# Kernel optimization log

Measured on AMD Instinct MI355X. Metric: run time of the kernel, lower is better.

Reference implementation:

```python
import jax, jax.numpy as jnp
import numpy as np

K_IN, K_OUT, K_STATE = 32, 32, 1024
BATCH, SEQ = 64, 512


def setup_inputs() -> dict:
    key = jax.random.key(0)
    ks = jax.random.split(key, 10)
    stdv = 1.0 / np.sqrt(K_STATE)
    u = lambda k, shape: jax.random.uniform(k, shape, jnp.float32, -stdv, stdv)
    return {
        "inputs": jax.random.normal(ks[0], (BATCH, SEQ, K_IN), jnp.float32),
        "state0": jnp.zeros((K_STATE,), jnp.float32),
        "W_e": u(ks[1], (K_STATE, K_IN)),
        "b_e": u(ks[2], (K_STATE,)),
        "W_ih": u(ks[3], (3 * K_STATE, K_STATE)),
        "b_ih": u(ks[4], (3 * K_STATE,)),
        "W_hh": u(ks[5], (3 * K_STATE, K_STATE)),
        "b_hh": u(ks[6], (3 * K_STATE,)),
        "W_ly": u(ks[7], (K_OUT, K_STATE)),
    }


def reference(inputs, state0, W_e, b_e, W_ih, b_ih, W_hh, b_hh, W_ly):
    # inputs: (B, T, k_in). interpol='constant' => x_half/x_full are unused by GRUCell.
    B, T, _ = inputs.shape
    H = W_hh.shape[1]
    # expand_input: tanh(Linear(k_in -> k_state)), batched over all timesteps
    xe = jnp.tanh(jnp.einsum('btk,hk->bth', inputs, W_e) + b_e)  # (B,T,H)
    # precompute input-side GRU gate projections in one big matmul
    xp = jnp.einsum('bth,gh->btg', xe, W_ih) + b_ih  # (B,T,3H)
    h0 = jnp.broadcast_to(state0, (B, H))

    def step(h, xp_t):
        gh = h @ W_hh.T + b_hh  # (B,3H)
        xr, xz, xn = jnp.split(xp_t, 3, axis=-1)
        hr, hz, hn = jnp.split(gh, 3, axis=-1)
        r = jax.nn.sigmoid(xr + hr)
        z = jax.nn.sigmoid(xz + hz)
        n = jnp.tanh(xn + r * hn)
        h_new = (1.0 - z) * n + z * h
        return h_new, h_new

    _, hs = jax.lax.scan(step, h0, jnp.swapaxes(xp, 0, 1))  # hs: (T,B,H)
    states = jnp.swapaxes(hs, 0, 1)  # (B,T,H)
    outputs = jnp.einsum('bth,oh->bto', states, W_ly)  # (B,T,k_out)
    return outputs, states
```

## Files before the change

kernel.cpp:

```cpp
#include <hip/hip_runtime.h>
#include <hip/hip_bf16.h>
#include <stdint.h>

typedef short short8 __attribute__((ext_vector_type(8)));
typedef float f32x4 __attribute__((ext_vector_type(4)));
typedef unsigned short u16;

__device__ __forceinline__ float bf2f(u16 b){ unsigned u = ((unsigned)b) << 16; float f; __builtin_memcpy(&f, &u, 4); return f; }
__device__ __forceinline__ u16 f2bf(float f){ unsigned u; __builtin_memcpy(&u, &f, 4); u = (u + 0x7fffu + ((u >> 16) & 1u)) >> 16; return (u16)u; }
__device__ __forceinline__ float sigm(float x){ return 1.f / (1.f + __expf(-x)); }
__device__ __forceinline__ float tanh_(float x){ float e = __expf(2.f * x); return 1.f - 2.f / (e + 1.f); }

__device__ __forceinline__ short8 ld_cohx4(const u16* p){
  short8 d;
  asm volatile("global_load_dwordx4 %0, %1, off sc0 sc1" : "=v"(d) : "v"(p) : "memory");
  return d;
}
__device__ __forceinline__ int ld_coh_u32(const int* p){
  int d;
  asm volatile("global_load_dword %0, %1, off sc0 sc1" : "=v"(d) : "v"(p) : "memory");
  return d;
}
__device__ __forceinline__ void st_coh_u16(u16* p, u16 v){
  asm volatile("global_store_short %0, %1, off sc0 sc1" :: "v"(p), "v"(v) : "memory");
}
__device__ __forceinline__ void st_coh_u32(int* p, int v){
  asm volatile("global_store_dword %0, %1, off sc0 sc1" :: "v"(p), "v"(v) : "memory");
}
__device__ __forceinline__ void wait_vm0(){ asm volatile("s_waitcnt vmcnt(0)" ::: "memory"); }

__global__ __launch_bounds__(256) void k_init(const float* __restrict__ Wih, const float* __restrict__ Whh,
                                              const float* __restrict__ s0,
                                              u16* __restrict__ Wihb, u16* __restrict__ Whhb,
                                              u16* __restrict__ hslab, int* __restrict__ flags)
{
  int i = blockIdx.x * 256 + threadIdx.x;
  int n = 3072 * 1024;
  for (int idx = i; idx < n; idx += gridDim.x * 256){
    Wihb[idx] = f2bf(Wih[idx]);
    Whhb[idx] = f2bf(Whh[idx]);
  }
  if (i < 65536){
    int k = ((i >> 8) & 63) * 16 + (i & 15);
    hslab[65536 + i] = f2bf(s0[k]);
  }
  if (i < 4 * 512 * 64) flags[i] = 0;
}

__global__ __launch_bounds__(256) void k_xe(const float* __restrict__ inp, const float* __restrict__ We,
                                            const float* __restrict__ be, u16* __restrict__ xe)
{
  __shared__ float si[64][32];
  size_t m0 = (size_t)blockIdx.x * 64;
  int tid = threadIdx.x;
  for (int i = tid; i < 2048; i += 256)
    si[i >> 5][i & 31] = inp[m0 * 32 + i];
  __syncthreads();
  #pragma unroll
  for (int jj = 0; jj < 4; ++jj){
    int j = jj * 256 + tid;
    f32x4 wr[8];
    #pragma unroll
    for (int q = 0; q < 8; ++q)
      wr[q] = *(const f32x4*)(We + (size_t)j * 32 + q * 4);
    float bias = be[j];
    for (int mi = 0; mi < 64; ++mi){
      float acc = bias;
      #pragma unroll
      for (int q = 0; q < 8; ++q){
        f32x4 x = *(const f32x4*)(&si[mi][q * 4]);
        acc += x[0]*wr[q][0] + x[1]*wr[q][1] + x[2]*wr[q][2] + x[3]*wr[q][3];
      }
      xe[(m0 + mi) * 1024 + j] = f2bf(tanh_(acc));
    }
  }
}

__global__ __launch_bounds__(256) void k_xp(const u16* __restrict__ A, const u16* __restrict__ Bw,
                                            const float* __restrict__ bias, u16* __restrict__ C)
{
  __shared__ u16 As[128 * 32];
  __shared__ u16 Bs[128 * 32];
  int tid = threadIdx.x, lane = tid & 63, wv = tid >> 6;
  int wr = wv >> 1, wc = wv & 1;
  int l15 = lane & 15, l4 = lane >> 4;
  int bid = blockIdx.x;
  int mb = bid / 24, nb = bid % 24;
  int m0 = mb * 128, n0 = nb * 128;

  int srow = lane >> 2, skk = (lane & 3) * 8;
  const u16* Ab = A + ((size_t)m0 + wv * 32 + srow) * 1024 + skk;
  const u16* Bb = Bw + ((size_t)n0 + wv * 32 + srow) * 1024 + skk;

  f32x4 acc[4][4] = {};
  for (int k0 = 0; k0 < 1024; k0 += 32){
    __syncthreads();
    __builtin_amdgcn_global_load_lds(Ab + k0,              &As[(wv * 2)     * 512], 16, 0, 0);
    __builtin_amdgcn_global_load_lds(Ab + k0 + 16 * 1024,  &As[(wv * 2 + 1) * 512], 16, 0, 0);
    __builtin_amdgcn_global_load_lds(Bb + k0,              &Bs[(wv * 2)     * 512], 16, 0, 0);
    __builtin_amdgcn_global_load_lds(Bb + k0 + 16 * 1024,  &Bs[(wv * 2 + 1) * 512], 16, 0, 0);
    __syncthreads();
    short8 af[4], bf[4];
    #pragma unroll
    for (int i = 0; i < 4; ++i){
      af[i] = *(const short8*)(As + (size_t)(wr * 64 + i * 16 + l15) * 32 + l4 * 8);
      bf[i] = *(const short8*)(Bs + (size_t)(wc * 64 + i * 16 + l15) * 32 + l4 * 8);
    }
    #pragma unroll
    for (int i = 0; i < 4; ++i)
      #pragma unroll
      for (int j = 0; j < 4; ++j)
        acc[i][j] = __builtin_amdgcn_mfma_f32_16x16x32_bf16(af[i], bf[j], acc[i][j], 0, 0, 0);
  }
  #pragma unroll
  for (int j = 0; j < 4; ++j){
    int n = n0 + wc * 64 + j * 16 + l15;
    float bv = bias[n];
    #pragma unroll
    for (int i = 0; i < 4; ++i){
      int mrow = m0 + wr * 64 + i * 16 + l4 * 4;
      #pragma unroll
      for (int r = 0; r < 4; ++r)
        C[(size_t)(mrow + r) * 3072 + n] = f2bf(acc[i][j][r] + bv);
    }
  }
}

__global__ __launch_bounds__(256, 1) void k_rec(const u16* __restrict__ Whhb, const float* __restrict__ bhh,
                                                const u16* __restrict__ xpb, const float* __restrict__ s0,
                                                u16* __restrict__ hslab, float* __restrict__ states,
                                                int* __restrict__ flags)
{
  int w = blockIdx.x;
  int g = w & 3;
  int s = w >> 2;
  int jb = s * 16;
  int tid = threadIdx.x, lane = tid & 63, wv = tid >> 6;
  int l15 = lane & 15, l4 = lane >> 4;

  short8 wreg[3][8];
  #pragma unroll
  for (int gt = 0; gt < 3; ++gt){
    const u16* wp = Whhb + (size_t)(gt * 1024 + jb + l15) * 1024 + wv * 256 + l4 * 8;
    #pragma unroll
    for (int ks = 0; ks < 8; ++ks)
      wreg[gt][ks] = *(const short8*)(wp + ks * 32);
  }
  float bb0 = bhh[jb + l15], bb1 = bhh[1024 + jb + l15], bb2 = bhh[2048 + jb + l15];
  float hreg[4];
  { float v = s0[jb + l15]; hreg[0] = hreg[1] = hreg[2] = hreg[3] = v; }

  __shared__ f32x4 part[3][3][64];

  for (int t = 0; t < 512; ++t){
    u16 xq[12];
    if (wv == 0){
      #pragma unroll
      for (int gt = 0; gt < 3; ++gt)
        #pragma unroll
        for (int r = 0; r < 4; ++r){
          int b = g * 16 + l4 * 4 + r;
          xq[gt * 4 + r] = xpb[((size_t)b * 512 + t) * 3072 + gt * 1024 + jb + l15];
        }
    }
    if (t > 0){
      const int* fp_ = flags + ((size_t)g * 512 + (t - 1)) * 64 + wv * 16 + l15;
      while (true){
        int v = ld_coh_u32(fp_);
        wait_vm0();
        if (__all(v != 0)) break;
        __builtin_amdgcn_s_sleep(1);
      }
      __builtin_amdgcn_sched_barrier(0);
    }
    int rbuf = (t & 1) ^ 1;
    const char* hs = (const char*)hslab + (((size_t)rbuf * 4 + g) * 64 + wv * 16) * 512;
    const char* hl = hs + l15 * 32 + (l4 & 1) * 16;
    short8 af[8];
    #pragma unroll
    for (int ks = 0; ks < 8; ++ks)
      af[ks] = ld_cohx4((const u16*)(hl + (ks * 2 + (l4 >> 1)) * 512));
    wait_vm0();
    __builtin_amdgcn_sched_barrier(0);
    f32x4 a0 = {}, a1 = {}, a2 = {};
    #pragma unroll
    for (int ks = 0; ks < 8; ++ks){
      a0 = __builtin_amdgcn_mfma_f32_16x16x32_bf16(af[ks], wreg[0][ks], a0, 0, 0, 0);
      a1 = __builtin_amdgcn_mfma_f32_16x16x32_bf16(af[ks], wreg[1][ks], a1, 0, 0, 0);
      a2 = __builtin_amdgcn_mfma_f32_16x16x32_bf16(af[ks], wreg[2][ks], a2, 0, 0, 0);
    }
    if (wv){
      part[wv - 1][0][lane] = a0;
      part[wv - 1][1][lane] = a1;
      part[wv - 1][2][lane] = a2;
    }
    __syncthreads();
    if (wv == 0){
      f32x4 g0 = a0 + part[0][0][lane] + part[1][0][lane] + part[2][0][lane];
      f32x4 g1 = a1 + part[0][1][lane] + part[1][1][lane] + part[2][1][lane];
      f32x4 g2 = a2 + part[0][2][lane] + part[1][2][lane] + part[2][2][lane];
      int wb = t & 1;
      float hn_[4];
      #pragma unroll
      for (int r = 0; r < 4; ++r){
        float rr = sigm(bf2f(xq[r])      + g0[r] + bb0);
        float zz = sigm(bf2f(xq[4 + r])  + g1[r] + bb1);
        float nn = tanh_(bf2f(xq[8 + r]) + rr * (g2[r] + bb2));
        hn_[r] = (1.f - zz) * nn + zz * hreg[r];
        hreg[r] = hn_[r];
      }
      u16* hw = hslab + (((size_t)wb * 4 + g) * 64 + s) * 256;
      #pragma unroll
      for (int r = 0; r < 4; ++r)
        st_coh_u16(hw + (l4 * 4 + r) * 16 + l15, f2bf(hn_[r]));
      wait_vm0();
      if (lane == 0)
        st_coh_u32(flags + ((size_t)g * 512 + t) * 64 + s, 1);
      #pragma unroll
      for (int r = 0; r < 4; ++r)
        states[((size_t)(g * 16 + l4 * 4 + r) * 512 + t) * 1024 + jb + l15] = hn_[r];
    }
  }
}

__global__ __launch_bounds__(256) void k_out(const float* __restrict__ st, const float* __restrict__ Wly,
                                             float* __restrict__ out)
{
  __shared__ float srow[8][1024];
  size_t m0 = (size_t)blockIdx.x * 8;
  int tid = threadIdx.x;
  for (int i = tid; i < 8 * 1024; i += 256)
    srow[i >> 10][i & 1023] = st[(m0 + (i >> 10)) * 1024 + (i & 1023)];
  __syncthreads();
  int mi = tid >> 5, o = tid & 31;
  const float* wp = Wly + (size_t)o * 1024;
  float acc = 0.f;
  #pragma unroll 4
  for (int k = 0; k < 1024; k += 4){
    f32x4 w = *(const f32x4*)(wp + k);
    f32x4 x = *(const f32x4*)(&srow[mi][k]);
    acc += x[0]*w[0] + x[1]*w[1] + x[2]*w[2] + x[3]*w[3];
  }
  out[(m0 + mi) * 32 + o] = acc;
}

extern "C" void kernel_launch(void* const* d_in, const int* in_sizes, int n_in,
                              void* d_out, int out_size, void* d_ws, size_t ws_size,
                              hipStream_t stream)
{
  const float* inputs = (const float*)d_in[0];
  const float* s0     = (const float*)d_in[1];
  const float* We     = (const float*)d_in[2];
  const float* be     = (const float*)d_in[3];
  const float* Wih    = (const float*)d_in[4];
  const float* bih    = (const float*)d_in[5];
  const float* Whh    = (const float*)d_in[6];
  const float* bhh    = (const float*)d_in[7];
  const float* Wly    = (const float*)d_in[8];

  float* out    = (float*)d_out;
  float* states = out + (size_t)64 * 512 * 32;

  char* ws = (char*)d_ws;
  u16* xe    = (u16*)ws;  ws += (size_t)32768 * 1024 * 2;
  u16* xpb   = (u16*)ws;  ws += (size_t)32768 * 3072 * 2;
  u16* Wihb  = (u16*)ws;  ws += (size_t)3072 * 1024 * 2;
  u16* Whhb  = (u16*)ws;  ws += (size_t)3072 * 1024 * 2;
  u16* hslab = (u16*)ws;  ws += (size_t)2 * 4 * 64 * 256 * 2;
  int* flags = (int*)ws;  ws += (size_t)4 * 512 * 64 * 4;

  k_init<<<dim3(4096), dim3(256), 0, stream>>>(Wih, Whh, s0, Wihb, Whhb, hslab, flags);
  k_xe<<<dim3(512), dim3(256), 0, stream>>>(inputs, We, be, xe);
  k_xp<<<dim3(6144), dim3(256), 0, stream>>>(xe, Wihb, bih, xpb);

  void* args[] = { (void*)&Whhb, (void*)&bhh, (void*)&xpb, (void*)&s0,
                   (void*)&hslab, (void*)&states, (void*)&flags };
  hipError_t e = hipLaunchCooperativeKernel((const void*)k_rec, dim3(256), dim3(256), args, 0, stream);
  if (e != hipSuccess){
    (void)hipGetLastError();
    k_rec<<<dim3(256), dim3(256), 0, stream>>>(Whhb, bhh, xpb, s0, hslab, states, flags);
  }
  k_out<<<dim3(4096), dim3(256), 0, stream>>>(states, Wly, out);
}
```

Before: 3.594 ms.

## Fuse input-gate projection into recurrent kernel, computing next step during the current one

Removes the separate xp GEMM kernel and its large bf16 intermediate buffer. Each recurrent block now computes the input-side gate projections for its 16 hidden units and 16 batch rows on the fly from xe and W_ih, double-buffered in shared memory and computed for step t+1 after step t's update. This avoids writing and re-reading about 200MB of xp. The cost is extra MFMA work and W_ih/xe loads inside the latency-critical serial loop, and keeping the partials in fp32 changes rounding slightly.

```diff
diff --git a/kernel.cpp b/kernel.cpp
--- a/kernel.cpp
+++ b/kernel.cpp
@@ -76,58 +76,9 @@
   }
 }
 
-__global__ __launch_bounds__(256) void k_xp(const u16* __restrict__ A, const u16* __restrict__ Bw,
-                                            const float* __restrict__ bias, u16* __restrict__ C)
-{
-  __shared__ u16 As[128 * 32];
-  __shared__ u16 Bs[128 * 32];
-  int tid = threadIdx.x, lane = tid & 63, wv = tid >> 6;
-  int wr = wv >> 1, wc = wv & 1;
-  int l15 = lane & 15, l4 = lane >> 4;
-  int bid = blockIdx.x;
-  int mb = bid / 24, nb = bid % 24;
-  int m0 = mb * 128, n0 = nb * 128;
-
-  int srow = lane >> 2, skk = (lane & 3) * 8;
-  const u16* Ab = A + ((size_t)m0 + wv * 32 + srow) * 1024 + skk;
-  const u16* Bb = Bw + ((size_t)n0 + wv * 32 + srow) * 1024 + skk;
-
-  f32x4 acc[4][4] = {};
-  for (int k0 = 0; k0 < 1024; k0 += 32){
-    __syncthreads();
-    __builtin_amdgcn_global_load_lds(Ab + k0,              &As[(wv * 2)     * 512], 16, 0, 0);
-    __builtin_amdgcn_global_load_lds(Ab + k0 + 16 * 1024,  &As[(wv * 2 + 1) * 512], 16, 0, 0);
-    __builtin_amdgcn_global_load_lds(Bb + k0,              &Bs[(wv * 2)     * 512], 16, 0, 0);
-    __builtin_amdgcn_global_load_lds(Bb + k0 + 16 * 1024,  &Bs[(wv * 2 + 1) * 512], 16, 0, 0);
-    __syncthreads();
-    short8 af[4], bf[4];
-    #pragma unroll
-    for (int i = 0; i < 4; ++i){
-      af[i] = *(const short8*)(As + (size_t)(wr * 64 + i * 16 + l15) * 32 + l4 * 8);
-      bf[i] = *(const short8*)(Bs + (size_t)(wc * 64 + i * 16 + l15) * 32 + l4 * 8);
-    }
-    #pragma unroll
-    for (int i = 0; i < 4; ++i)
-      #pragma unroll
-      for (int j = 0; j < 4; ++j)
-        acc[i][j] = __builtin_amdgcn_mfma_f32_16x16x32_bf16(af[i], bf[j], acc[i][j], 0, 0, 0);
-  }
-  #pragma unroll
-  for (int j = 0; j < 4; ++j){
-    int n = n0 + wc * 64 + j * 16 + l15;
-    float bv = bias[n];
-    #pragma unroll
-    for (int i = 0; i < 4; ++i){
-      int mrow = m0 + wr * 64 + i * 16 + l4 * 4;
-      #pragma unroll
-      for (int r = 0; r < 4; ++r)
-        C[(size_t)(mrow + r) * 3072 + n] = f2bf(acc[i][j][r] + bv);
-    }
-  }
-}
-
-__global__ __launch_bounds__(256, 1) void k_rec(const u16* __restrict__ Whhb, const float* __restrict__ bhh,
-                                                const u16* __restrict__ xpb, const float* __restrict__ s0,
+__global__ __launch_bounds__(256, 1) void k_rec(const u16* __restrict__ Whhb, const u16* __restrict__ Wihb,
+                                                const float* __restrict__ bhh, const float* __restrict__ bih,
+                                                const u16* __restrict__ xe, const float* __restrict__ s0,
                                                 u16* __restrict__ hslab, float* __restrict__ states,
                                                 int* __restrict__ flags)
 {
@@ -147,22 +98,40 @@
       wreg[gt][ks] = *(const short8*)(wp + ks * 32);
   }
   float bb0 = bhh[jb + l15], bb1 = bhh[1024 + jb + l15], bb2 = bhh[2048 + jb + l15];
+  float bi0 = bih[jb + l15], bi1 = bih[1024 + jb + l15], bi2 = bih[2048 + jb + l15];
   float hreg[4];
   { float v = s0[jb + l15]; hreg[0] = hreg[1] = hreg[2] = hreg[3] = v; }
 
+  const u16* wih0 = Wihb + (size_t)(jb + l15) * 1024 + wv * 256 + l4 * 8;
+  const u16* wih1 = wih0 + (size_t)1024 * 1024;
+  const u16* wih2 = wih1 + (size_t)1024 * 1024;
+  const u16* xeb = xe + ((size_t)(g * 16 + l15) * 512) * 1024 + wv * 256 + l4 * 8;
+
   __shared__ f32x4 part[3][3][64];
+  __shared__ f32x4 xpart[2][3][3][64];
+  f32x4 cx0, cx1, cx2;
+
+  {
+    const u16* xp_ = xeb;
+    short8 ax[8];
+    #pragma unroll
+    for (int ks = 0; ks < 8; ++ks) ax[ks] = *(const short8*)(xp_ + ks * 32);
+    f32x4 x0 = {}, x1 = {}, x2 = {};
+    #pragma unroll
+    for (int ks = 0; ks < 8; ++ks){
+      short8 w0 = *(const short8*)(wih0 + ks * 32);
+      short8 w1 = *(const short8*)(wih1 + ks * 32);
+      short8 w2 = *(const short8*)(wih2 + ks * 32);
+      x0 = __builtin_amdgcn_mfma_f32_16x16x32_bf16(ax[ks], w0, x0, 0, 0, 0);
+      x1 = __builtin_amdgcn_mfma_f32_16x16x32_bf16(ax[ks], w1, x1, 0, 0, 0);
+      x2 = __builtin_amdgcn_mfma_f32_16x16x32_bf16(ax[ks], w2, x2, 0, 0, 0);
+    }
+    if (wv){ xpart[0][wv - 1][0][lane] = x0; xpart[0][wv - 1][1][lane] = x1; xpart[0][wv - 1][2][lane] = x2; }
+    else   { cx0 = x0; cx1 = x1; cx2 = x2; }
+  }
+  __syncthreads();
 
   for (int t = 0; t < 512; ++t){
-    u16 xq[12];
-    if (wv == 0){
-      #pragma unroll
-      for (int gt = 0; gt < 3; ++gt)
-        #pragma unroll
-        for (int r = 0; r < 4; ++r){
-          int b = g * 16 + l4 * 4 + r;
-          xq[gt * 4 + r] = xpb[((size_t)b * 512 + t) * 3072 + gt * 1024 + jb + l15];
-        }
-    }
     if (t > 0){
       const int* fp_ = flags + ((size_t)g * 512 + (t - 1)) * 64 + wv * 16 + l15;
       while (true){
@@ -199,13 +168,17 @@
       f32x4 g0 = a0 + part[0][0][lane] + part[1][0][lane] + part[2][0][lane];
       f32x4 g1 = a1 + part[0][1][lane] + part[1][1][lane] + part[2][1][lane];
       f32x4 g2 = a2 + part[0][2][lane] + part[1][2][lane] + part[2][2][lane];
+      int pb = t & 1;
+      f32x4 x0s = cx0 + xpart[pb][0][0][lane] + xpart[pb][1][0][lane] + xpart[pb][2][0][lane];
+      f32x4 x1s = cx1 + xpart[pb][0][1][lane] + xpart[pb][1][1][lane] + xpart[pb][2][1][lane];
+      f32x4 x2s = cx2 + xpart[pb][0][2][lane] + xpart[pb][1][2][lane] + xpart[pb][2][2][lane];
       int wb = t & 1;
       float hn_[4];
       #pragma unroll
       for (int r = 0; r < 4; ++r){
-        float rr = sigm(bf2f(xq[r])      + g0[r] + bb0);
-        float zz = sigm(bf2f(xq[4 + r])  + g1[r] + bb1);
-        float nn = tanh_(bf2f(xq[8 + r]) + rr * (g2[r] + bb2));
+        float rr = sigm(x0s[r] + bi0 + g0[r] + bb0);
+        float zz = sigm(x1s[r] + bi1 + g1[r] + bb1);
+        float nn = tanh_(x2s[r] + bi2 + rr * (g2[r] + bb2));
         hn_[r] = (1.f - zz) * nn + zz * hreg[r];
         hreg[r] = hn_[r];
       }
@@ -219,6 +192,25 @@
       #pragma unroll
       for (int r = 0; r < 4; ++r)
         states[((size_t)(g * 16 + l4 * 4 + r) * 512 + t) * 1024 + jb + l15] = hn_[r];
+    }
+    if (t + 1 < 512){
+      const u16* xp_ = xeb + (size_t)(t + 1) * 1024;
+      short8 ax[8];
+      #pragma unroll
+      for (int ks = 0; ks < 8; ++ks) ax[ks] = *(const short8*)(xp_ + ks * 32);
+      f32x4 x0 = {}, x1 = {}, x2 = {};
+      #pragma unroll
+      for (int ks = 0; ks < 8; ++ks){
+        short8 w0 = *(const short8*)(wih0 + ks * 32);
+        short8 w1 = *(const short8*)(wih1 + ks * 32);
+        short8 w2 = *(const short8*)(wih2 + ks * 32);
+        x0 = __builtin_amdgcn_mfma_f32_16x16x32_bf16(ax[ks], w0, x0, 0, 0, 0);
+        x1 = __builtin_amdgcn_mfma_f32_16x16x32_bf16(ax[ks], w1, x1, 0, 0, 0);
+        x2 = __builtin_amdgcn_mfma_f32_16x16x32_bf16(ax[ks], w2, x2, 0, 0, 0);
+      }
+      int pb = (t + 1) & 1;
+      if (wv){ xpart[pb][wv - 1][0][lane] = x0; xpart[pb][wv - 1][1][lane] = x1; xpart[pb][wv - 1][2][lane] = x2; }
+      else   { cx0 = x0; cx1 = x1; cx2 = x2; }
     }
   }
 }
@@ -263,7 +255,6 @@
 
   char* ws = (char*)d_ws;
   u16* xe    = (u16*)ws;  ws += (size_t)32768 * 1024 * 2;
-  u16* xpb   = (u16*)ws;  ws += (size_t)32768 * 3072 * 2;
   u16* Wihb  = (u16*)ws;  ws += (size_t)3072 * 1024 * 2;
   u16* Whhb  = (u16*)ws;  ws += (size_t)3072 * 1024 * 2;
   u16* hslab = (u16*)ws;  ws += (size_t)2 * 4 * 64 * 256 * 2;
@@ -271,14 +262,13 @@
 
   k_init<<<dim3(4096), dim3(256), 0, stream>>>(Wih, Whh, s0, Wihb, Whhb, hslab, flags);
   k_xe<<<dim3(512), dim3(256), 0, stream>>>(inputs, We, be, xe);
-  k_xp<<<dim3(6144), dim3(256), 0, stream>>>(xe, Wihb, bih, xpb);
-
-  void* args[] = { (void*)&Whhb, (void*)&bhh, (void*)&xpb, (void*)&s0,
+
+  void* args[] = { (void*)&Whhb, (void*)&Wihb, (void*)&bhh, (void*)&bih, (void*)&xe, (void*)&s0,
                    (void*)&hslab, (void*)&states, (void*)&flags };
   hipError_t e = hipLaunchCooperativeKernel((const void*)k_rec, dim3(256), dim3(256), args, 0, stream);
   if (e != hipSuccess){
     (void)hipGetLastError();
-    k_rec<<<dim3(256), dim3(256), 0, stream>>>(Whhb, bhh, xpb, s0, hslab, states, flags);
+    k_rec<<<dim3(256), dim3(256), 0, stream>>>(Whhb, Wihb, bhh, bih, xe, s0, hslab, states, flags);
   }
   k_out<<<dim3(4096), dim3(256), 0, stream>>>(states, Wly, out);
 }
```

Measured after the change: 3.367 ms. 1.07x faster.
